# Kernel optimization log

Measured on AMD Instinct MI355X. Metric: run time of the kernel, lower is better.

## Reference

```python
import jax, jax.numpy as jnp
import numpy as np

D_MODEL = 1024
NUM_HEADS = 16
HEAD_DIM = D_MODEL // NUM_HEADS


def setup_inputs() -> dict:
    key = jax.random.key(0)
    ks = jax.random.split(key, 9)
    B, S = 2, 2048
    s = 1.0 / np.sqrt(D_MODEL)
    return {
        "x": jax.random.normal(ks[0], (B, S, D_MODEL), dtype=jnp.float32),
        "Wq": jax.random.normal(ks[1], (D_MODEL, D_MODEL), dtype=jnp.float32) * s,
        "bq": jnp.zeros((D_MODEL,), dtype=jnp.float32),
        "Wk": jax.random.normal(ks[2], (D_MODEL, D_MODEL), dtype=jnp.float32) * s,
        "bk": jnp.zeros((D_MODEL,), dtype=jnp.float32),
        "Wv": jax.random.normal(ks[3], (D_MODEL, D_MODEL), dtype=jnp.float32) * s,
        "bv": jnp.zeros((D_MODEL,), dtype=jnp.float32),
        "Wo": jax.random.normal(ks[4], (D_MODEL, D_MODEL), dtype=jnp.float32) * s,
        "bo": jnp.zeros((D_MODEL,), dtype=jnp.float32),
    }


def reference(x, Wq, bq, Wk, bk, Wv, bv, Wo, bo):
    B, S, _ = x.shape
    # projections; weights stored as (in, out) so y = x @ W + b
    def heads(y):  # [B,S,D] -> [B,H,S,Dh]
        return y.reshape(B, S, NUM_HEADS, HEAD_DIM).transpose(0, 2, 1, 3)

    Q = heads(x @ Wq + bq)
    K = heads(x @ Wk + bk)
    V = heads(x @ Wv + bv)
    scale = 1.0 / np.sqrt(HEAD_DIM).astype(np.float32)
    scores = jnp.einsum("bhqd,bhkd->bhqk", Q, K) * scale  # [B,H,S,S]
    attn = jax.nn.softmax(scores, axis=-1)
    ctx = jnp.einsum("bhqk,bhkd->bhqd", attn, V)  # [B,H,S,Dh]
    ctx = ctx.transpose(0, 2, 1, 3).reshape(B, S, D_MODEL)
    return ctx @ Wo + bo
```

## Files before the change

kernel.cpp:

```cpp
#include <hip/hip_runtime.h>
#include <hip/hip_bf16.h>

#define SEQ   2048
#define NH    16
#define HD    64
#define DM    1024
#define MROWS 4096

#define QSCALE 0.1803368801111204f

typedef __attribute__((ext_vector_type(4))) float f32x4;
typedef __attribute__((ext_vector_type(8))) short s16x8;
typedef __attribute__((ext_vector_type(4))) short s16x4;

__device__ __forceinline__ short f2bf(float f) {
  union { float f; unsigned u; } v; v.f = f;
  return (short)((v.u + 0x7fff + ((v.u >> 16) & 1)) >> 16);
}

__device__ __forceinline__ unsigned pack2bf(float lo, float hi) {
  unsigned ul = __float_as_uint(lo) + 0x8000u;
  unsigned uh = __float_as_uint(hi) + 0x8000u;
  return __builtin_amdgcn_perm(uh, ul, 0x07060302u);
}

__device__ __forceinline__ void gload_lds16(const short* g, short* l) {
  __builtin_amdgcn_global_load_lds(
      (const __attribute__((address_space(1))) void*)g,
      (__attribute__((address_space(3))) void*)l, 16, 0, 0);
}

#define SWZ(row, gg) ((((row) << 3) + (((gg) ^ ((row) & 7)))) << 3)
#define SWZ16(row, gg) ((((row) << 4) + (((gg) ^ ((row) & 15)))) << 3)

__global__ void prep(const float* __restrict__ x, short* __restrict__ xb,
                     const float* __restrict__ Wq, const float* __restrict__ Wk,
                     const float* __restrict__ Wv, const float* __restrict__ Wo,
                     short* __restrict__ WT) {
  const int t = threadIdx.x;
  if (blockIdx.z == 4) {
    int c = blockIdx.y * 16 + blockIdx.x;
    #pragma unroll
    for (int itr = 0; itr < 8; ++itr) {
      int i = c * 16384 + itr * 2048 + t * 8;
      const float4* p = reinterpret_cast<const float4*>(x + i);
      float4 a = p[0], b = p[1];
      s16x8 o;
      o[0] = f2bf(a.x); o[1] = f2bf(a.y); o[2] = f2bf(a.z); o[3] = f2bf(a.w);
      o[4] = f2bf(b.x); o[5] = f2bf(b.y); o[6] = f2bf(b.z); o[7] = f2bf(b.w);
      *reinterpret_cast<s16x8*>(xb + i) = o;
    }
    return;
  }
  __shared__ float tile[64][65];
  const float* W = (blockIdx.z == 0) ? Wq : (blockIdx.z == 1) ? Wk : (blockIdx.z == 2) ? Wv : Wo;
  short* dst = WT + (size_t)blockIdx.z * DM * DM;
  int kbase = blockIdx.x * 64;
  int nbase = blockIdx.y * 64;
  {
    int n4 = (t & 15) * 4;
    #pragma unroll
    for (int rr = 0; rr < 4; ++rr) {
      int r = (t >> 4) + 16 * rr;
      float4 v = *reinterpret_cast<const float4*>(W + (size_t)(kbase + r) * DM + nbase + n4);
      tile[r][n4] = v.x; tile[r][n4 + 1] = v.y; tile[r][n4 + 2] = v.z; tile[r][n4 + 3] = v.w;
    }
  }
  __syncthreads();
  {
    int n = t >> 2, kc = (t & 3) * 16;
    short tmp[16];
    #pragma unroll
    for (int j = 0; j < 16; ++j) tmp[j] = f2bf(tile[kc + j][n]);
    s16x8* q = reinterpret_cast<s16x8*>(dst + (size_t)(nbase + n) * DM + kbase + kc);
    q[0] = *reinterpret_cast<s16x8*>(tmp);
    q[1] = *reinterpret_cast<s16x8*>(tmp + 8);
  }
}

__global__ __launch_bounds__(256, 2) void gemm_qkv(
    const short* __restrict__ A, const short* __restrict__ BT,
    const float* __restrict__ bias0, const float* __restrict__ bias1,
    const float* __restrict__ bias2,
    short* __restrict__ oQ, short* __restrict__ oK, short* __restrict__ oVt) {
  __shared__ __align__(16) short As[128 * 64];
  __shared__ __align__(16) short Bs[128 * 64];
  const int lin = blockIdx.x;
  const int wg = (lin & 7) * 96 + (lin >> 3);
  const int bx = wg & 31;
  const int by = wg >> 5;
  const int lane = threadIdx.x & 63;
  const int wid = threadIdx.x >> 6;
  const int q15 = lane & 15, g4 = lane >> 4;
  const int mbase = bx * 128;
  const int nbase = by * 128;
  const int wm = wid >> 1, wn = wid & 1;

  f32x4 acc[4][4] = {};
  const int srow = lane >> 3;
  const int sg = (lane & 7) ^ srow;

  for (int k0 = 0; k0 < DM; k0 += 64) {
    #pragma unroll
    for (int j = 0; j < 4; ++j) {
      int c = wid * 4 + j;
      int row = c * 8 + srow;
      gload_lds16(A + (size_t)(mbase + row) * DM + k0 + sg * 8, As + c * 512);
      gload_lds16(BT + (size_t)(nbase + row) * DM + k0 + sg * 8, Bs + c * 512);
    }
    __syncthreads();
    #pragma unroll
    for (int ks = 0; ks < 2; ++ks) {
      s16x8 af[4], bfr[4];
      #pragma unroll
      for (int m = 0; m < 4; ++m)
        af[m] = *reinterpret_cast<const s16x8*>(As + SWZ(wm * 64 + m * 16 + q15, ks * 4 + g4));
      #pragma unroll
      for (int n = 0; n < 4; ++n)
        bfr[n] = *reinterpret_cast<const s16x8*>(Bs + SWZ(wn * 64 + n * 16 + q15, ks * 4 + g4));
      #pragma unroll
      for (int m = 0; m < 4; ++m)
        #pragma unroll
        for (int n = 0; n < 4; ++n)
          acc[m][n] = __builtin_amdgcn_mfma_f32_16x16x32_bf16(af[m], bfr[n], acc[m][n], 0, 0, 0);
    }
    __syncthreads();
  }

  const int r0 = mbase + wm * 64;
  const int c0 = nbase + wn * 64;
  #pragma unroll
  for (int m = 0; m < 4; ++m) {
    #pragma unroll
    for (int n = 0; n < 4; ++n) {
      int rr = r0 + m * 16 + g4 * 4;
      int cc = c0 + n * 16 + q15;
      int seg = cc >> 10, c1 = cc & 1023;
      const float* bp = (seg == 0) ? bias0 : (seg == 1) ? bias1 : bias2;
      float bv = bp[c1];
      int h = c1 >> 6, d = c1 & 63;
      if (seg == 2) {
        s16x4 o;
        #pragma unroll
        for (int i = 0; i < 4; ++i) o[i] = f2bf(acc[m][n][i] + bv);
        int b = rr >> 11, s = rr & 2047;
        *reinterpret_cast<s16x4*>(
            oVt + ((size_t)(b * NH + h) * HD + d) * SEQ + s) = o;
      } else {
        short* dst = (seg == 0) ? oQ : oK;
        #pragma unroll
        for (int i = 0; i < 4; ++i) {
          int r = rr + i;
          float v = acc[m][n][i] + bv;
          if (seg == 0) v *= QSCALE;
          int b = r >> 11, s = r & 2047;
          size_t idx = (((size_t)(b * NH + h) * SEQ + s) << 6) + d;
          dst[idx] = f2bf(v);
        }
      }
    }
  }
}

__global__ __launch_bounds__(256, 2) void gemm_o(
    const short* __restrict__ A, const short* __restrict__ BT,
    const float* __restrict__ bias, float* __restrict__ oF) {
  __shared__ __align__(16) short As[64 * 128];
  __shared__ __align__(16) short Bs[128 * 128];
  const int lin = blockIdx.x;
  const int wg = (lin & 7) * 64 + (lin >> 3);
  const int bx = wg & 63;
  const int by = wg >> 6;
  const int lane = threadIdx.x & 63;
  const int wid = threadIdx.x >> 6;
  const int q15 = lane & 15, g4 = lane >> 4;
  const int mbase = bx * 64;
  const int nbase = by * 128;
  const int t = threadIdx.x;
  const int wbase = t & 448;

  f32x4 acc[4][2] = {};

  for (int k0 = 0; k0 < DM; k0 += 128) {
    #pragma unroll
    for (int l = 0; l < 4; ++l) {
      int glin = l * 256 + t;
      int row = glin >> 4, gg = glin & 15;
      int sgg = gg ^ (row & 15);
      gload_lds16(A + (size_t)(mbase + row) * DM + k0 + sgg * 8,
                  As + (l * 256 + wbase) * 8);
    }
    #pragma unroll
    for (int l = 0; l < 8; ++l) {
      int glin = l * 256 + t;
      int row = glin >> 4, gg = glin & 15;
      int sgg = gg ^ (row & 15);
      gload_lds16(BT + (size_t)(nbase + row) * DM + k0 + sgg * 8,
                  Bs + (l * 256 + wbase) * 8);
    }
    __syncthreads();
    #pragma unroll
    for (int ks = 0; ks < 4; ++ks) {
      s16x8 af[4], bfr[2];
      #pragma unroll
      for (int m = 0; m < 4; ++m)
        af[m] = *reinterpret_cast<const s16x8*>(As + SWZ16(m * 16 + q15, ks * 4 + g4));
      #pragma unroll
      for (int n = 0; n < 2; ++n)
        bfr[n] = *reinterpret_cast<const s16x8*>(Bs + SWZ16(wid * 32 + n * 16 + q15, ks * 4 + g4));
      #pragma unroll
      for (int m = 0; m < 4; ++m)
        #pragma unroll
        for (int n = 0; n < 2; ++n)
          acc[m][n] = __builtin_amdgcn_mfma_f32_16x16x32_bf16(af[m], bfr[n], acc[m][n], 0, 0, 0);
    }
    __syncthreads();
  }

  #pragma unroll
  for (int m = 0; m < 4; ++m) {
    #pragma unroll
    for (int n = 0; n < 2; ++n) {
      int cc = nbase + wid * 32 + n * 16 + q15;
      float bv = bias[cc];
      #pragma unroll
      for (int i = 0; i < 4; ++i) {
        int r = mbase + m * 16 + g4 * 4 + i;
        oF[(size_t)r * DM + cc] = acc[m][n][i] + bv;
      }
    }
  }
}

__global__ __launch_bounds__(512, 4) void attn(const short* __restrict__ Q,
                                               const short* __restrict__ K,
                                               const short* __restrict__ Vt,
                                               short* __restrict__ ctx) {
  const int lin = blockIdx.x;
  const int xcd = lin & 7, idx = lin >> 3;
  const int bh = xcd * 4 + (idx >> 4);
  const int qt = idx & 15;
  const int lane = threadIdx.x & 63;
  const int wid = threadIdx.x >> 6;
  const int q15 = lane & 15, g4 = lane >> 4;
  const int qrow = qt * 128 + wid * 16;
  const short* Qh = Q + (size_t)bh * SEQ * HD;
  const short* Kh = K + (size_t)bh * SEQ * HD;
  const short* Vh = Vt + (size_t)bh * HD * SEQ;

  __shared__ __align__(16) short Ks[2][64 * 64];
  __shared__ __align__(16) short Vs[2][64 * 64];
  __shared__ __align__(16) short Plds[8][16][72];
  short(*P)[72] = Plds[wid];

  const int t = threadIdx.x;
  const int srow = t >> 3;
  const int sg = (t & 7) ^ (srow & 7);
  const short* ksrc = Kh + (size_t)srow * HD + sg * 8;
  const short* vsrc = Vh + (size_t)srow * SEQ + sg * 8;

  s16x8 qf[2];
  #pragma unroll
  for (int ks = 0; ks < 2; ++ks)
    qf[ks] = *reinterpret_cast<const s16x8*>(
        Qh + (size_t)(qrow + q15) * HD + ks * 32 + g4 * 8);

  s16x8 ones;
  #pragma unroll
  for (int i = 0; i < 8; ++i) ones[i] = (short)0x3F80;

  f32x4 acco[4] = {};
  f32x4 lacc = {};
  float mrun = 0.f;

  gload_lds16(ksrc, Ks[0] + wid * 512);
  gload_lds16(vsrc, Vs[0] + wid * 512);
  __syncthreads();

  int cur = 0;
  for (int it = 0; it < SEQ / 64; ++it) {
    if (it + 1 < SEQ / 64) {
      gload_lds16(ksrc + (size_t)(it + 1) * 64 * HD, Ks[cur ^ 1] + wid * 512);
      gload_lds16(vsrc + (it + 1) * 64, Vs[cur ^ 1] + wid * 512);
    }
    const short* Kb = Ks[cur];
    const short* Vb = Vs[cur];

    f32x4 sacc[4] = {};
    #pragma unroll
    for (int kb = 0; kb < 4; ++kb) {
      s16x8 kf0 = *reinterpret_cast<const s16x8*>(Kb + SWZ(kb * 16 + q15, g4));
      s16x8 kf1 = *reinterpret_cast<const s16x8*>(Kb + SWZ(kb * 16 + q15, g4 + 4));
      sacc[kb] = __builtin_amdgcn_mfma_f32_16x16x32_bf16(kf0, qf[0], sacc[kb], 0, 0, 0);
      sacc[kb] = __builtin_amdgcn_mfma_f32_16x16x32_bf16(kf1, qf[1], sacc[kb], 0, 0, 0);
    }

    if (it == 0) {
      float t0 = fmaxf(fmaxf(sacc[0][0], sacc[0][1]), fmaxf(sacc[0][2], sacc[0][3]));
      float t1 = fmaxf(fmaxf(sacc[1][0], sacc[1][1]), fmaxf(sacc[1][2], sacc[1][3]));
      float t2 = fmaxf(fmaxf(sacc[2][0], sacc[2][1]), fmaxf(sacc[2][2], sacc[2][3]));
      float t3 = fmaxf(fmaxf(sacc[3][0], sacc[3][1]), fmaxf(sacc[3][2], sacc[3][3]));
      float tmax = fmaxf(fmaxf(t0, t1), fmaxf(t2, t3));
      float tm = fmaxf(tmax, __shfl_xor(tmax, 16));
      mrun = fmaxf(tm, __shfl_xor(tm, 32));
    }

    #pragma unroll
    for (int kb = 0; kb < 4; ++kb) {
      float p0 = __builtin_amdgcn_exp2f(sacc[kb][0] - mrun);
      float p1 = __builtin_amdgcn_exp2f(sacc[kb][1] - mrun);
      float p2 = __builtin_amdgcn_exp2f(sacc[kb][2] - mrun);
      float p3 = __builtin_amdgcn_exp2f(sacc[kb][3] - mrun);
      uint2 w;
      w.x = pack2bf(p0, p1);
      w.y = pack2bf(p2, p3);
      *reinterpret_cast<uint2*>(&P[q15][kb * 16 + g4 * 4]) = w;
    }
    s16x8 pf0 = *reinterpret_cast<const s16x8*>(&P[q15][g4 * 8]);
    s16x8 pf1 = *reinterpret_cast<const s16x8*>(&P[q15][32 + g4 * 8]);

    lacc = __builtin_amdgcn_mfma_f32_16x16x32_bf16(ones, pf0, lacc, 0, 0, 0);
    lacc = __builtin_amdgcn_mfma_f32_16x16x32_bf16(ones, pf1, lacc, 0, 0, 0);

    #pragma unroll
    for (int dvb = 0; dvb < 4; ++dvb) {
      s16x8 vf0 = *reinterpret_cast<const s16x8*>(Vb + SWZ(dvb * 16 + q15, g4));
      s16x8 vf1 = *reinterpret_cast<const s16x8*>(Vb + SWZ(dvb * 16 + q15, g4 + 4));
      acco[dvb] = __builtin_amdgcn_mfma_f32_16x16x32_bf16(vf0, pf0, acco[dvb], 0, 0, 0);
      acco[dvb] = __builtin_amdgcn_mfma_f32_16x16x32_bf16(vf1, pf1, acco[dvb], 0, 0, 0);
    }

    __syncthreads();
    cur ^= 1;
  }

  const int b = bh >> 4, h = bh & 15;
  float inv = 1.f / lacc[0];
  int q = qrow + q15;
  #pragma unroll
  for (int dvb = 0; dvb < 4; ++dvb) {
    s16x4 o;
    #pragma unroll
    for (int i = 0; i < 4; ++i) o[i] = f2bf(acco[dvb][i] * inv);
    int d = dvb * 16 + g4 * 4;
    *reinterpret_cast<s16x4*>(ctx + ((size_t)b * SEQ + q) * DM + h * HD + d) = o;
  }
}

extern "C" void kernel_launch(void* const* d_in, const int* in_sizes, int n_in,
                              void* d_out, int out_size, void* d_ws, size_t ws_size,
                              hipStream_t stream) {
  const float* x = (const float*)d_in[0];
  const float* Wq = (const float*)d_in[1];
  const float* bq = (const float*)d_in[2];
  const float* Wk = (const float*)d_in[3];
  const float* bk = (const float*)d_in[4];
  const float* Wv = (const float*)d_in[5];
  const float* bv = (const float*)d_in[6];
  const float* Wo = (const float*)d_in[7];
  const float* bo = (const float*)d_in[8];

  char* ws = (char*)d_ws;
  const size_t MB8 = (size_t)8 << 20;
  short* xb  = (short*)(ws);
  short* WT  = (short*)(ws + 1 * MB8);
  short* Qb  = (short*)(ws + 2 * MB8);
  short* Kb  = (short*)(ws + 3 * MB8);
  short* Vtb = (short*)(ws + 5 * MB8);
  short* ctx = (short*)(ws + 6 * MB8);

  prep<<<dim3(16, 16, 5), 256, 0, stream>>>(x, xb, Wq, Wk, Wv, Wo, WT);
  gemm_qkv<<<dim3(768), 256, 0, stream>>>(xb, WT, bq, bk, bv, Qb, Kb, Vtb);
  attn<<<dim3(512), 512, 0, stream>>>(Qb, Kb, Vtb, ctx);
  gemm_o<<<dim3(512), 256, 0, stream>>>(ctx, WT + (size_t)3072 * DM, bo, (float*)d_out);
}
```

Measured before the change: 116.2 us.

## Process K/V tiles in pairs with four-slot LDS ring and swizzled P buffer

```diff
diff --git a/kernel.cpp b/kernel.cpp
--- a/kernel.cpp
+++ b/kernel.cpp
@@ -248,10 +248,11 @@
   const short* Kh = K + (size_t)bh * SEQ * HD;
   const short* Vh = Vt + (size_t)bh * HD * SEQ;
 
-  __shared__ __align__(16) short Ks[2][64 * 64];
-  __shared__ __align__(16) short Vs[2][64 * 64];
-  __shared__ __align__(16) short Plds[8][16][72];
-  short(*P)[72] = Plds[wid];
+  __shared__ __align__(16) short Ks[4][64 * 64];
+  __shared__ __align__(16) short Vs[4][64 * 64];
+  __shared__ __align__(16) short Plds[8][16 * 64];
+  char* Pw = (char*)Plds[wid];
+  const unsigned pswz = (unsigned)((q15 & 7) << 4);
 
   const int t = threadIdx.x;
   const int srow = t >> 3;
@@ -273,19 +274,14 @@
   f32x4 lacc = {};
   float mrun = 0.f;
 
-  gload_lds16(ksrc, Ks[0] + wid * 512);
-  gload_lds16(vsrc, Vs[0] + wid * 512);
-  __syncthreads();
-
-  int cur = 0;
-  for (int it = 0; it < SEQ / 64; ++it) {
-    if (it + 1 < SEQ / 64) {
-      gload_lds16(ksrc + (size_t)(it + 1) * 64 * HD, Ks[cur ^ 1] + wid * 512);
-      gload_lds16(vsrc + (it + 1) * 64, Vs[cur ^ 1] + wid * 512);
-    }
-    const short* Kb = Ks[cur];
-    const short* Vb = Vs[cur];
-
+  auto pf = [&](int tile, int slot) {
+    if (tile < SEQ / 64) {
+      gload_lds16(ksrc + (size_t)tile * 64 * HD, Ks[slot] + wid * 512);
+      gload_lds16(vsrc + tile * 64, Vs[slot] + wid * 512);
+    }
+  };
+
+  auto step = [&](const short* Kb, const short* Vb, bool seed) {
     f32x4 sacc[4] = {};
     #pragma unroll
     for (int kb = 0; kb < 4; ++kb) {
@@ -294,8 +290,7 @@
       sacc[kb] = __builtin_amdgcn_mfma_f32_16x16x32_bf16(kf0, qf[0], sacc[kb], 0, 0, 0);
       sacc[kb] = __builtin_amdgcn_mfma_f32_16x16x32_bf16(kf1, qf[1], sacc[kb], 0, 0, 0);
     }
-
-    if (it == 0) {
+    if (seed) {
       float t0 = fmaxf(fmaxf(sacc[0][0], sacc[0][1]), fmaxf(sacc[0][2], sacc[0][3]));
       float t1 = fmaxf(fmaxf(sacc[1][0], sacc[1][1]), fmaxf(sacc[1][2], sacc[1][3]));
       float t2 = fmaxf(fmaxf(sacc[2][0], sacc[2][1]), fmaxf(sacc[2][2], sacc[2][3]));
@@ -304,7 +299,6 @@
       float tm = fmaxf(tmax, __shfl_xor(tmax, 16));
       mrun = fmaxf(tm, __shfl_xor(tm, 32));
     }
-
     #pragma unroll
     for (int kb = 0; kb < 4; ++kb) {
       float p0 = __builtin_amdgcn_exp2f(sacc[kb][0] - mrun);
@@ -314,14 +308,15 @@
       uint2 w;
       w.x = pack2bf(p0, p1);
       w.y = pack2bf(p2, p3);
-      *reinterpret_cast<uint2*>(&P[q15][kb * 16 + g4 * 4]) = w;
-    }
-    s16x8 pf0 = *reinterpret_cast<const s16x8*>(&P[q15][g4 * 8]);
-    s16x8 pf1 = *reinterpret_cast<const s16x8*>(&P[q15][32 + g4 * 8]);
-
+      unsigned wb = (unsigned)(q15 * 128 + kb * 32 + g4 * 8) ^ pswz;
+      *reinterpret_cast<uint2*>(Pw + wb) = w;
+    }
+    unsigned rb0 = (unsigned)(q15 * 128 + g4 * 16) ^ pswz;
+    unsigned rb1 = (unsigned)(q15 * 128 + 64 + g4 * 16) ^ pswz;
+    s16x8 pf0 = *reinterpret_cast<const s16x8*>(Pw + rb0);
+    s16x8 pf1 = *reinterpret_cast<const s16x8*>(Pw + rb1);
     lacc = __builtin_amdgcn_mfma_f32_16x16x32_bf16(ones, pf0, lacc, 0, 0, 0);
     lacc = __builtin_amdgcn_mfma_f32_16x16x32_bf16(ones, pf1, lacc, 0, 0, 0);
-
     #pragma unroll
     for (int dvb = 0; dvb < 4; ++dvb) {
       s16x8 vf0 = *reinterpret_cast<const s16x8*>(Vb + SWZ(dvb * 16 + q15, g4));
@@ -329,9 +324,24 @@
       acco[dvb] = __builtin_amdgcn_mfma_f32_16x16x32_bf16(vf0, pf0, acco[dvb], 0, 0, 0);
       acco[dvb] = __builtin_amdgcn_mfma_f32_16x16x32_bf16(vf1, pf1, acco[dvb], 0, 0, 0);
     }
-
-    __syncthreads();
-    cur ^= 1;
+  };
+
+  pf(0, 0);
+  pf(1, 1);
+  __syncthreads();
+
+  for (int m = 0; m < SEQ / 256; ++m) {
+    int t0 = 4 * m;
+    pf(t0 + 2, 2);
+    pf(t0 + 3, 3);
+    step(Ks[0], Vs[0], m == 0);
+    step(Ks[1], Vs[1], false);
+    __syncthreads();
+    pf(t0 + 4, 0);
+    pf(t0 + 5, 1);
+    step(Ks[2], Vs[2], false);
+    step(Ks[3], Vs[3], false);
+    __syncthreads();
   }
 
   const int b = bh >> 4, h = bh & 15;
```

Result: faster. 110.8 us (median of 2 runs) (-4.6%).
